# Optimization experiments

Hardware: AMD Instinct MI355X
Metric: run time of the kernel (lower is better)

The kernel has to match this reference:

```python
import jax, jax.numpy as jnp
import numpy as np


def _pairwise_dist(x, y):
    # x: [B, N, D], y: [B, M, D] -> [B, N, M] Euclidean distances.
    # Use ||x||^2 + ||y||^2 - 2<x,y> (gram form) to avoid the [B,N,M,D]
    # broadcast intermediate the torch code materializes.
    x2 = jnp.sum(x * x, axis=-1)  # [B, N]
    y2 = jnp.sum(y * y, axis=-1)  # [B, M]
    xy = jnp.einsum('bnd,bmd->bnm', x, y)  # [B, N, M]
    sq = x2[:, :, None] + y2[:, None, :] - 2.0 * xy
    return jnp.sqrt(jnp.maximum(sq, 1e-12))


def setup_inputs() -> dict:
    key = jax.random.key(0)
    k1, k2 = jax.random.split(key)
    B, N, M, D = 8, 4096, 4096, 64
    pred = jax.random.normal(k1, (B, N, D), dtype=jnp.float32)
    label = jax.random.normal(k2, (B, M, D), dtype=jnp.float32)
    return {"pred": pred, "label": label}


def reference(pred, label):
    dis = _pairwise_dist(pred, label)  # [B, N, M]
    dis_xy = jnp.max(jnp.min(dis, axis=2))  # max over all (b, n) of min over m
    dis_yx = jnp.max(jnp.min(dis, axis=1))  # max over all (b, m) of min over n
    return dis_xy + dis_yx
```

## Files before the change

kernel.cpp:

```cpp
#include <hip/hip_runtime.h>
#include <hip/hip_bf16.h>

#define B_ 8
#define N_ 4096
#define M_ 4096
#define D_ 64
#define BNT (B_ * N_)
#define BMT (B_ * M_)
#define TILE 128
#define CHUNK_TILES 8
#define NCHUNK (M_ / (TILE * CHUNK_TILES))

typedef short bf16x8 __attribute__((ext_vector_type(8)));
typedef float f32x4 __attribute__((ext_vector_type(4)));

__device__ __forceinline__ unsigned short f2bf(float f) {
  __hip_bfloat16 h = __float2bfloat16(f);
  return *reinterpret_cast<unsigned short*>(&h);
}

__device__ __forceinline__ unsigned fkey(float f) {
  unsigned b = __float_as_uint(f);
  return b ^ ((unsigned)((int)b >> 31) | 0x80000000u);
}
__device__ __forceinline__ float funkey(unsigned k) {
  unsigned b = (k & 0x80000000u) ? (k ^ 0x80000000u) : ~k;
  return __uint_as_float(b);
}

__device__ __forceinline__ void gload_lds16(const void* g, void* l) {
  __builtin_amdgcn_global_load_lds(
      (const __attribute__((address_space(1))) unsigned int*)g,
      (__attribute__((address_space(3))) unsigned int*)l, 16, 0, 0);
}

template <bool BF>
__device__ __forceinline__ void stage_tile(const void* gsrc, unsigned short* lds,
                                           int t, int srcpat) {
  if (BF) {
    const char* gp = (const char*)gsrc;
    int w = t >> 6;
#pragma unroll
    for (int i = 0; i < 4; i++) {
      int q = w * 4 + i;
      gload_lds16(gp + q * 1024 + srcpat, (char*)lds + q * 1024);
    }
  } else {
    const float4* g4 = (const float4*)gsrc;
#pragma unroll
    for (int i = 0; i < 8; i++) {
      int off = i * 256 + t;
      float4 v = g4[off];
      int row = off >> 4;
      int cb = (off & 15) * 8;
      int ba = (row * 128 + cb) ^ ((row & 7) << 4);
      ushort4 p;
      p.x = f2bf(v.x); p.y = f2bf(v.y); p.z = f2bf(v.z); p.w = f2bf(v.w);
      *(ushort4*)((char*)lds + ba) = p;
    }
  }
}

template <bool CONV>
__global__ __launch_bounds__(256) void prep_kernel(
    const float* __restrict__ pred, const float* __restrict__ label,
    unsigned short* __restrict__ predbf, unsigned short* __restrict__ labelbf,
    float* __restrict__ x2, float* __restrict__ y2,
    unsigned* __restrict__ minN, unsigned* __restrict__ minM,
    unsigned* __restrict__ gmax) {
  int t = threadIdx.x;
  int lane = t & 15;
  long row = (long)blockIdx.x * 16 + (t >> 4);
  const float4* src;
  unsigned short* bdst;
  float* ndst;
  unsigned* mdst;
  if (row < BNT) {
    src = (const float4*)(pred + row * D_);
    bdst = predbf + row * D_;
    ndst = x2 + row;
    mdst = minN + row;
  } else {
    long r2 = row - BNT;
    src = (const float4*)(label + r2 * D_);
    bdst = labelbf + r2 * D_;
    ndst = y2 + r2;
    mdst = minM + r2;
  }
  float4 v = src[lane];
  if (CONV) {
    ushort4 p;
    p.x = f2bf(v.x); p.y = f2bf(v.y); p.z = f2bf(v.z); p.w = f2bf(v.w);
    *(ushort4*)(bdst + lane * 4) = p;
  }
  float s = v.x * v.x + v.y * v.y + v.z * v.z + v.w * v.w;
  s += __shfl_xor(s, 1);
  s += __shfl_xor(s, 2);
  s += __shfl_xor(s, 4);
  s += __shfl_xor(s, 8);
  if (lane == 0) {
    *ndst = s;
    *mdst = 0xFFFFFFFFu;
  }
  if (blockIdx.x == 0 && t < 2) gmax[t] = 0u;
}

template <bool BF>
__global__ __launch_bounds__(256) void pass_kernel(
    const void* __restrict__ Asrc,
    const void* __restrict__ Bsrc,
    const float* __restrict__ normB,
    unsigned* __restrict__ minOut) {
  __shared__ alignas(16) unsigned short As[TILE * 64];
  __shared__ alignas(16) unsigned short Bs[TILE * 64];

  const int t = threadIdx.x;
  const int b = blockIdx.z;
  const int a0 = blockIdx.x * TILE;
  const int w = t >> 6, l = t & 63;
  const int g = l >> 4, c = l & 15;

  const int srcpat = (l >> 3) * 128 + (((l & 7) * 16) ^ ((l >> 3) << 4));

  const size_t rowbytes = BF ? 128 : 256;
  const char* Agl = (const char*)Asrc + ((size_t)b * N_ + a0) * rowbytes;
  const char* Bgl = (const char*)Bsrc + (size_t)b * M_ * rowbytes;

  stage_tile<BF>(Agl, As, t, srcpat);
  stage_tile<BF>(Bgl + (size_t)(blockIdx.y * CHUNK_TILES) * TILE * rowbytes, Bs, t, srcpat);
  __syncthreads();

  bf16x8 af[2][2];
#pragma unroll
  for (int kk = 0; kk < 2; kk++)
#pragma unroll
    for (int mi = 0; mi < 2; mi++) {
      int r = w * 32 + mi * 16 + c;
      int ba = (r * 128 + kk * 64 + g * 16) ^ ((r & 7) << 4);
      af[kk][mi] = *(const bf16x8*)((const char*)As + ba);
    }

  float rmin[2][4];
#pragma unroll
  for (int mi = 0; mi < 2; mi++)
#pragma unroll
    for (int e = 0; e < 4; e++) rmin[mi][e] = INFINITY;

  for (int it = 0; it < CHUNK_TILES; it++) {
    const int m0 = (blockIdx.y * CHUNK_TILES + it) * TILE;

    float nbv[8];
#pragma unroll
    for (int ni = 0; ni < 8; ni++)
      nbv[ni] = normB[(size_t)b * M_ + m0 + ni * 16 + c];

    f32x4 acc[2][8];
#pragma unroll
    for (int kk = 0; kk < 2; kk++) {
      bf16x8 bfr[8];
#pragma unroll
      for (int ni = 0; ni < 8; ni++) {
        int r = ni * 16 + c;
        int ba = (r * 128 + kk * 64 + g * 16) ^ ((r & 7) << 4);
        bfr[ni] = *(const bf16x8*)((const char*)Bs + ba);
      }
#pragma unroll
      for (int mi = 0; mi < 2; mi++)
#pragma unroll
        for (int ni = 0; ni < 8; ni++) {
          if (kk == 0)
            acc[mi][ni] = __builtin_amdgcn_mfma_f32_16x16x32_bf16(
                af[0][mi], bfr[ni], (f32x4){0.f, 0.f, 0.f, 0.f}, 0, 0, 0);
          else
            acc[mi][ni] = __builtin_amdgcn_mfma_f32_16x16x32_bf16(
                af[1][mi], bfr[ni], acc[mi][ni], 0, 0, 0);
        }
    }
    __syncthreads();

    if (it + 1 < CHUNK_TILES)
      stage_tile<BF>(Bgl + (size_t)(blockIdx.y * CHUNK_TILES + it + 1) * TILE * rowbytes,
                     Bs, t, srcpat);

#pragma unroll
    for (int mi = 0; mi < 2; mi++)
#pragma unroll
      for (int ni = 0; ni < 8; ni++)
#pragma unroll
        for (int e = 0; e < 4; e++)
          rmin[mi][e] = fminf(rmin[mi][e], fmaf(-2.f, acc[mi][ni][e], nbv[ni]));

    __syncthreads();
  }

#pragma unroll
  for (int mi = 0; mi < 2; mi++)
#pragma unroll
    for (int e = 0; e < 4; e++) {
      float r = rmin[mi][e];
      r = fminf(r, __shfl_xor(r, 1));
      r = fminf(r, __shfl_xor(r, 2));
      r = fminf(r, __shfl_xor(r, 4));
      r = fminf(r, __shfl_xor(r, 8));
      rmin[mi][e] = r;
    }
  if (c == 0) {
#pragma unroll
    for (int mi = 0; mi < 2; mi++)
#pragma unroll
      for (int e = 0; e < 4; e++) {
        int row = a0 + w * 32 + mi * 16 + g * 4 + e;
        atomicMin(&minOut[(size_t)b * N_ + row], fkey(rmin[mi][e]));
      }
  }
}

__global__ __launch_bounds__(256) void final1_kernel(
    const unsigned* __restrict__ minN, const unsigned* __restrict__ minM,
    const float* __restrict__ x2, const float* __restrict__ y2,
    unsigned* __restrict__ gmax) {
  int dir = blockIdx.x >> 6;
  int blk = blockIdx.x & 63;
  const unsigned* src = dir ? minM : minN;
  const float* nrm = dir ? y2 : x2;
  size_t base = (size_t)blk * 512;
  float mx = -INFINITY;
  for (int i = threadIdx.x; i < 512; i += 256)
    mx = fmaxf(mx, nrm[base + i] + funkey(src[base + i]));
#pragma unroll
  for (int mask = 1; mask < 64; mask <<= 1) mx = fmaxf(mx, __shfl_xor(mx, mask));
  __shared__ float sm[4];
  if ((threadIdx.x & 63) == 0) sm[threadIdx.x >> 6] = mx;
  __syncthreads();
  if (threadIdx.x == 0) {
    mx = fmaxf(fmaxf(sm[0], sm[1]), fmaxf(sm[2], sm[3]));
    atomicMax(&gmax[dir], fkey(mx));
  }
}

__global__ void final2_kernel(const unsigned* __restrict__ gmax, float* __restrict__ out) {
  if (threadIdx.x == 0)
    out[0] = sqrtf(fmaxf(funkey(gmax[0]), 1e-12f)) +
             sqrtf(fmaxf(funkey(gmax[1]), 1e-12f));
}

extern "C" void kernel_launch(void* const* d_in, const int* in_sizes, int n_in,
                              void* d_out, int out_size, void* d_ws, size_t ws_size,
                              hipStream_t stream) {
  const float* pred = (const float*)d_in[0];
  const float* label = (const float*)d_in[1];
  char* ws = (char*)d_ws;

  const size_t bfBytes = (size_t)BNT * D_ * 2;
  const size_t needFast = 2 * bfBytes + (size_t)(BNT + BMT) * 8 + 64;

  if (ws_size >= needFast) {
    unsigned short* predbf = (unsigned short*)ws;
    unsigned short* labelbf = (unsigned short*)(ws + bfBytes);
    float* x2 = (float*)(ws + 2 * bfBytes);
    float* y2 = x2 + BNT;
    unsigned* minN = (unsigned*)(y2 + BMT);
    unsigned* minM = minN + BNT;
    unsigned* gmax = minM + BMT;

    prep_kernel<true><<<(BNT + BMT) / 16, 256, 0, stream>>>(
        pred, label, predbf, labelbf, x2, y2, minN, minM, gmax);
    pass_kernel<true><<<dim3(N_ / TILE, NCHUNK, B_), 256, 0, stream>>>(
        predbf, labelbf, y2, minN);
    pass_kernel<true><<<dim3(M_ / TILE, NCHUNK, B_), 256, 0, stream>>>(
        labelbf, predbf, x2, minM);
    final1_kernel<<<128, 256, 0, stream>>>(minN, minM, x2, y2, gmax);
    final2_kernel<<<1, 64, 0, stream>>>(gmax, (float*)d_out);
  } else {
    float* x2 = (float*)ws;
    float* y2 = x2 + BNT;
    unsigned* minN = (unsigned*)(y2 + BMT);
    unsigned* minM = minN + BNT;
    unsigned* gmax = minM + BMT;

    prep_kernel<false><<<(BNT + BMT) / 16, 256, 0, stream>>>(
        pred, label, nullptr, nullptr, x2, y2, minN, minM, gmax);
    pass_kernel<false><<<dim3(N_ / TILE, NCHUNK, B_), 256, 0, stream>>>(
        pred, label, y2, minN);
    pass_kernel<false><<<dim3(M_ / TILE, NCHUNK, B_), 256, 0, stream>>>(
        label, pred, x2, minM);
    final1_kernel<<<128, 256, 0, stream>>>(minN, minM, x2, y2, gmax);
    final2_kernel<<<1, 64, 0, stream>>>(gmax, (float*)d_out);
  }
}
```

Measured before the change: 63.32 us.

## Fuse both direction passes into one kernel computing row and column minima

Replaces the two separate pass kernels, which each recomputed the full pairwise gram, with one fused kernel. It computes each tile's dot products once and updates both the per-pred row minima and the per-label column minima. B tiles are double-buffered in LDS so the next tile's load overlaps the current compute, and the A tile shrinks to 64 rows with each wave taking 32 B columns. This halves the matrix-multiply work and global reads, at the cost of many more atomicMin operations on the column minima and extra shuffles.

After: 66.20 us. 4.5% more time.

```diff
diff --git a/kernel.cpp b/kernel.cpp
--- a/kernel.cpp
+++ b/kernel.cpp
@@ -7,9 +7,10 @@
 #define D_ 64
 #define BNT (B_ * N_)
 #define BMT (B_ * M_)
-#define TILE 128
+#define TA 64
+#define TB 128
 #define CHUNK_TILES 8
-#define NCHUNK (M_ / (TILE * CHUNK_TILES))
+#define MCHUNK (M_ / (TB * CHUNK_TILES))
 
 typedef short bf16x8 __attribute__((ext_vector_type(8)));
 typedef float f32x4 __attribute__((ext_vector_type(4)));
@@ -34,21 +35,22 @@
       (__attribute__((address_space(3))) unsigned int*)l, 16, 0, 0);
 }
 
-template <bool BF>
+template <int ROWS, bool BF>
 __device__ __forceinline__ void stage_tile(const void* gsrc, unsigned short* lds,
                                            int t, int srcpat) {
   if (BF) {
+    constexpr int PER_WAVE = (ROWS * 128 / 1024) / 4;
     const char* gp = (const char*)gsrc;
     int w = t >> 6;
 #pragma unroll
-    for (int i = 0; i < 4; i++) {
-      int q = w * 4 + i;
+    for (int i = 0; i < PER_WAVE; i++) {
+      int q = w * PER_WAVE + i;
       gload_lds16(gp + q * 1024 + srcpat, (char*)lds + q * 1024);
     }
   } else {
     const float4* g4 = (const float4*)gsrc;
 #pragma unroll
-    for (int i = 0; i < 8; i++) {
+    for (int i = 0; i < ROWS * 16 / 256; i++) {
       int off = i * 256 + t;
       float4 v = g4[off];
       int row = off >> 4;
@@ -106,95 +108,95 @@
 }
 
 template <bool BF>
-__global__ __launch_bounds__(256) void pass_kernel(
-    const void* __restrict__ Asrc,
-    const void* __restrict__ Bsrc,
-    const float* __restrict__ normB,
-    unsigned* __restrict__ minOut) {
-  __shared__ alignas(16) unsigned short As[TILE * 64];
-  __shared__ alignas(16) unsigned short Bs[TILE * 64];
+__global__ __launch_bounds__(256) void fused_kernel(
+    const void* __restrict__ Asrc, const void* __restrict__ Bsrc,
+    const float* __restrict__ x2g, const float* __restrict__ y2g,
+    unsigned* __restrict__ minN, unsigned* __restrict__ minM) {
+  __shared__ alignas(16) unsigned short As[TA * 64];
+  __shared__ alignas(16) unsigned short Bs[2][TB * 64];
+  __shared__ float red[4][TA];
 
   const int t = threadIdx.x;
   const int b = blockIdx.z;
-  const int a0 = blockIdx.x * TILE;
+  const int a0 = blockIdx.x * TA;
+  const int tile0 = blockIdx.y * CHUNK_TILES;
   const int w = t >> 6, l = t & 63;
   const int g = l >> 4, c = l & 15;
-
   const int srcpat = (l >> 3) * 128 + (((l & 7) * 16) ^ ((l >> 3) << 4));
 
   const size_t rowbytes = BF ? 128 : 256;
   const char* Agl = (const char*)Asrc + ((size_t)b * N_ + a0) * rowbytes;
   const char* Bgl = (const char*)Bsrc + (size_t)b * M_ * rowbytes;
 
-  stage_tile<BF>(Agl, As, t, srcpat);
-  stage_tile<BF>(Bgl + (size_t)(blockIdx.y * CHUNK_TILES) * TILE * rowbytes, Bs, t, srcpat);
+  stage_tile<TA, BF>(Agl, As, t, srcpat);
+  stage_tile<TB, BF>(Bgl + (size_t)tile0 * TB * rowbytes, Bs[0], t, srcpat);
   __syncthreads();
 
-  bf16x8 af[2][2];
+  bf16x8 af[2][4];
 #pragma unroll
   for (int kk = 0; kk < 2; kk++)
 #pragma unroll
-    for (int mi = 0; mi < 2; mi++) {
-      int r = w * 32 + mi * 16 + c;
+    for (int mi = 0; mi < 4; mi++) {
+      int r = mi * 16 + c;
       int ba = (r * 128 + kk * 64 + g * 16) ^ ((r & 7) << 4);
       af[kk][mi] = *(const bf16x8*)((const char*)As + ba);
     }
 
-  float rmin[2][4];
-#pragma unroll
-  for (int mi = 0; mi < 2; mi++)
+  float x2v[4][4];
+#pragma unroll
+  for (int mi = 0; mi < 4; mi++)
+#pragma unroll
+    for (int e = 0; e < 4; e++)
+      x2v[mi][e] = x2g[(size_t)b * N_ + a0 + mi * 16 + g * 4 + e];
+
+  float rmin[4][4];
+#pragma unroll
+  for (int mi = 0; mi < 4; mi++)
 #pragma unroll
     for (int e = 0; e < 4; e++) rmin[mi][e] = INFINITY;
 
   for (int it = 0; it < CHUNK_TILES; it++) {
-    const int m0 = (blockIdx.y * CHUNK_TILES + it) * TILE;
-
-    float nbv[8];
-#pragma unroll
-    for (int ni = 0; ni < 8; ni++)
-      nbv[ni] = normB[(size_t)b * M_ + m0 + ni * 16 + c];
-
-    f32x4 acc[2][8];
-#pragma unroll
-    for (int kk = 0; kk < 2; kk++) {
-      bf16x8 bfr[8];
-#pragma unroll
-      for (int ni = 0; ni < 8; ni++) {
-        int r = ni * 16 + c;
-        int ba = (r * 128 + kk * 64 + g * 16) ^ ((r & 7) << 4);
-        bfr[ni] = *(const bf16x8*)((const char*)Bs + ba);
-      }
-#pragma unroll
-      for (int mi = 0; mi < 2; mi++)
-#pragma unroll
-        for (int ni = 0; ni < 8; ni++) {
-          if (kk == 0)
-            acc[mi][ni] = __builtin_amdgcn_mfma_f32_16x16x32_bf16(
-                af[0][mi], bfr[ni], (f32x4){0.f, 0.f, 0.f, 0.f}, 0, 0, 0);
-          else
-            acc[mi][ni] = __builtin_amdgcn_mfma_f32_16x16x32_bf16(
-                af[1][mi], bfr[ni], acc[mi][ni], 0, 0, 0);
+    if (it + 1 < CHUNK_TILES)
+      stage_tile<TB, BF>(Bgl + (size_t)(tile0 + it + 1) * TB * rowbytes,
+                         Bs[(it + 1) & 1], t, srcpat);
+    const char* Bcur = (const char*)Bs[it & 1];
+    const int mrow_base = (tile0 + it) * TB + w * 32;
+
+#pragma unroll
+    for (int ni = 0; ni < 2; ni++) {
+      float nbv = y2g[(size_t)b * M_ + mrow_base + ni * 16 + c];
+      int r = w * 32 + ni * 16 + c;
+      bf16x8 b0 = *(const bf16x8*)(Bcur + ((r * 128 + g * 16) ^ ((r & 7) << 4)));
+      bf16x8 b1 = *(const bf16x8*)(Bcur + ((r * 128 + 64 + g * 16) ^ ((r & 7) << 4)));
+      f32x4 acc[4];
+#pragma unroll
+      for (int mi = 0; mi < 4; mi++)
+        acc[mi] = __builtin_amdgcn_mfma_f32_16x16x32_bf16(
+            af[0][mi], b0, (f32x4){0.f, 0.f, 0.f, 0.f}, 0, 0, 0);
+#pragma unroll
+      for (int mi = 0; mi < 4; mi++)
+        acc[mi] = __builtin_amdgcn_mfma_f32_16x16x32_bf16(
+            af[1][mi], b1, acc[mi], 0, 0, 0);
+
+      float cm = INFINITY;
+#pragma unroll
+      for (int mi = 0; mi < 4; mi++)
+#pragma unroll
+        for (int e = 0; e < 4; e++) {
+          float m2 = -2.f * acc[mi][e];
+          rmin[mi][e] = fminf(rmin[mi][e], m2 + nbv);
+          cm = fminf(cm, m2 + x2v[mi][e]);
         }
+      cm = fminf(cm, __shfl_xor(cm, 16));
+      cm = fminf(cm, __shfl_xor(cm, 32));
+      if (g == 0)
+        atomicMin(&minM[(size_t)b * M_ + mrow_base + ni * 16 + c], fkey(cm));
     }
     __syncthreads();
-
-    if (it + 1 < CHUNK_TILES)
-      stage_tile<BF>(Bgl + (size_t)(blockIdx.y * CHUNK_TILES + it + 1) * TILE * rowbytes,
-                     Bs, t, srcpat);
-
-#pragma unroll
-    for (int mi = 0; mi < 2; mi++)
-#pragma unroll
-      for (int ni = 0; ni < 8; ni++)
-#pragma unroll
-        for (int e = 0; e < 4; e++)
-          rmin[mi][e] = fminf(rmin[mi][e], fmaf(-2.f, acc[mi][ni][e], nbv[ni]));
-
-    __syncthreads();
-  }
-
-#pragma unroll
-  for (int mi = 0; mi < 2; mi++)
+  }
+
+#pragma unroll
+  for (int mi = 0; mi < 4; mi++)
 #pragma unroll
     for (int e = 0; e < 4; e++) {
       float r = rmin[mi][e];
@@ -206,12 +208,15 @@
     }
   if (c == 0) {
 #pragma unroll
-    for (int mi = 0; mi < 2; mi++)
-#pragma unroll
-      for (int e = 0; e < 4; e++) {
-        int row = a0 + w * 32 + mi * 16 + g * 4 + e;
-        atomicMin(&minOut[(size_t)b * N_ + row], fkey(rmin[mi][e]));
-      }
+    for (int mi = 0; mi < 4; mi++)
+#pragma unroll
+      for (int e = 0; e < 4; e++)
+        red[w][mi * 16 + g * 4 + e] = rmin[mi][e];
+  }
+  __syncthreads();
+  if (t < TA) {
+    float m = fminf(fminf(red[0][t], red[1][t]), fminf(red[2][t], red[3][t]));
+    atomicMin(&minN[(size_t)b * N_ + a0 + t], fkey(m));
   }
 }
 
@@ -265,10 +270,8 @@
 
     prep_kernel<true><<<(BNT + BMT) / 16, 256, 0, stream>>>(
         pred, label, predbf, labelbf, x2, y2, minN, minM, gmax);
-    pass_kernel<true><<<dim3(N_ / TILE, NCHUNK, B_), 256, 0, stream>>>(
-        predbf, labelbf, y2, minN);
-    pass_kernel<true><<<dim3(M_ / TILE, NCHUNK, B_), 256, 0, stream>>>(
-        labelbf, predbf, x2, minM);
+    fused_kernel<true><<<dim3(N_ / TA, MCHUNK, B_), 256, 0, stream>>>(
+        predbf, labelbf, x2, y2, minN, minM);
     final1_kernel<<<128, 256, 0, stream>>>(minN, minM, x2, y2, gmax);
     final2_kernel<<<1, 64, 0, stream>>>(gmax, (float*)d_out);
   } else {
@@ -280,10 +283,8 @@
 
     prep_kernel<false><<<(BNT + BMT) / 16, 256, 0, stream>>>(
         pred, label, nullptr, nullptr, x2, y2, minN, minM, gmax);
-    pass_kernel<false><<<dim3(N_ / TILE, NCHUNK, B_), 256, 0, stream>>>(
-        pred, label, y2, minN);
-    pass_kernel<false><<<dim3(M_ / TILE, NCHUNK, B_), 256, 0, stream>>>(
-        label, pred, x2, minM);
+    fused_kernel<false><<<dim3(N_ / TA, MCHUNK, B_), 256, 0, stream>>>(
+        pred, label, x2, y2, minN, minM);
     final1_kernel<<<128, 256, 0, stream>>>(minN, minM, x2, y2, gmax);
     final2_kernel<<<1, 64, 0, stream>>>(gmax, (float*)d_out);
   }
```
